# Optimization experiments

Hardware: AMD Instinct MI355X
Metric: run time of the kernel (lower is better)

Reference implementation:

```python
import jax, jax.numpy as jnp
import numpy as np

B, N, C = 8, 16384, 256

def setup_inputs() -> dict:
    key = jax.random.key(0)
    ks = jax.random.split(key, 5)
    scale = 1.0 / np.sqrt(C)
    return {
        "x_in": jax.random.normal(ks[0], (B, N, C), dtype=jnp.float32),
        "Wq": jax.random.normal(ks[1], (C, C), dtype=jnp.float32) * scale,
        "bq": jax.random.normal(ks[2], (C,), dtype=jnp.float32) * scale,
        "Wk": jax.random.normal(ks[3], (C, C), dtype=jnp.float32) * scale,
        "bk": jax.random.normal(ks[4], (C,), dtype=jnp.float32) * scale,
    }

def reference(x_in, Wq, bq, Wk, bk):
    b, n, c = x_in.shape
    # Faithful to torch: reshape (NOT transpose) to [B, C, N]
    x = x_in.reshape(b, c, n)
    # 1x1 Conv1d == per-position linear over channel dim
    Q = jnp.einsum('oc,bcn->bon', Wq, x) + bq[None, :, None]  # [B,C,N]
    K = jnp.einsum('oc,bcn->bon', Wk, x) + bk[None, :, None]  # [B,C,N]
    # Q @ K^T over length axis -> channel-channel scores [B,C,C]
    scores = jnp.einsum('bcn,bdn->bcd', Q, K)
    c_c = jax.nn.softmax(scores, axis=-1)
    # x_in @ c_c + residual -> [B,N,C]
    return jnp.einsum('bnc,bcd->bnd', x_in, c_c) + x_in
```

## Files before the change

### kernel.cpp

```cpp
#include <hip/hip_runtime.h>

#define Bn 8
#define Nn 16384
#define Cn 256
#define NC 32
#define CHUNK 512
#define NSTG 16

typedef __attribute__((ext_vector_type(4)))  float f32x4;
typedef __attribute__((ext_vector_type(16))) float f32x16;
typedef __attribute__((ext_vector_type(8)))  __bf16 bf16x8;
typedef __attribute__((ext_vector_type(8)))  _Float16 f16x8;
typedef __attribute__((ext_vector_type(8)))  unsigned short u16x8;

static __device__ __forceinline__ unsigned short f2bf(float f) {
    unsigned int u = __float_as_uint(f);
    u += 0x7fff + ((u >> 16) & 1);
    return (unsigned short)(u >> 16);
}
static __device__ __forceinline__ unsigned short f2h(float f) {
    return __builtin_bit_cast(unsigned short, (_Float16)f);
}
static __device__ __forceinline__ f32x16 mfma16h(u16x8 a, u16x8 b, f32x16 c) {
    return __builtin_amdgcn_mfma_f32_32x32x16_f16(
        __builtin_bit_cast(f16x8, a), __builtin_bit_cast(f16x8, b), c, 0, 0, 0);
}
static __device__ __forceinline__ f32x16 mfma16b(u16x8 a, u16x8 b, f32x16 c) {
    return __builtin_amdgcn_mfma_f32_32x32x16_bf16(
        __builtin_bit_cast(bf16x8, a), __builtin_bit_cast(bf16x8, b), c, 0, 0, 0);
}

__global__ __launch_bounds__(512, 4) void k_gram(
    const float* __restrict__ x, float* __restrict__ gpart,
    float* __restrict__ spart) {
  const int blk  = blockIdx.x;
  const int half = blk & 1;
  const int ck   = (blk >> 1) & (NC - 1);
  const int b    = blk >> 6;
  const float* xb = x + (size_t)b * Cn * Nn + (size_t)ck * CHUNK;
  const int rot  = (2 * ck + half) & (NSTG - 1);

  __shared__ __align__(16) char smem[2 * 20480];

  const int t    = threadIdx.x;
  const int lane = t & 63;
  const int w    = t >> 6;
  const int wm   = w & 1;
  const int wn   = w >> 1;
  const int ln   = lane & 31;
  const int kh   = lane >> 5;

  const int rt = t >> 3;
  const int c4 = t & 7;

  f32x16 acc[2][2];
#pragma unroll
  for (int m = 0; m < 2; ++m)
#pragma unroll
    for (int n = 0; n < 2; ++n)
#pragma unroll
      for (int i = 0; i < 16; ++i) acc[m][n][i] = 0.f;

  float srow[4] = {0.f, 0.f, 0.f, 0.f};
  const float* xrt = xb + (size_t)rt * Nn + c4 * 4;

  f32x4 ld[4];
  {
    const int sp = rot;
#pragma unroll
    for (int j = 0; j < 4; ++j)
      ld[j] = *(const f32x4*)(xrt + (size_t)j * (64 * Nn) + sp * 32);
  }

  for (int s = 0; s < NSTG; ++s) {
    char* buf = smem + (s & 1) * 20480;
#pragma unroll
    for (int j = 0; j < 4; ++j) {
      f32x4 v = ld[j];
      srow[j] += v.x + v.y + v.z + v.w;
      ushort4 h = make_ushort4(f2h(v.x), f2h(v.y), f2h(v.z), f2h(v.w));
      int row = rt + 64 * j;
      *(ushort4*)(buf + row * 80 + c4 * 8) = h;
    }
    if (s + 1 < NSTG) {
      const int sp = (s + 1 + rot) & (NSTG - 1);
#pragma unroll
      for (int j = 0; j < 4; ++j)
        ld[j] = *(const f32x4*)(xrt + (size_t)j * (64 * Nn) + sp * 32);
    }
    __syncthreads();
#pragma unroll
    for (int ks = 0; ks < 2; ++ks) {
      const int sl = ks * 2 + kh;
      u16x8 A[2], Bv[2];
#pragma unroll
      for (int m = 0; m < 2; ++m) {
        int r = half * 128 + wm * 64 + m * 32 + ln;
        A[m] = *(const u16x8*)(buf + r * 80 + sl * 16);
      }
#pragma unroll
      for (int n = 0; n < 2; ++n) {
        int r = wn * 64 + n * 32 + ln;
        Bv[n] = *(const u16x8*)(buf + r * 80 + sl * 16);
      }
#pragma unroll
      for (int m = 0; m < 2; ++m)
#pragma unroll
        for (int n = 0; n < 2; ++n)
          acc[m][n] = mfma16h(A[m], Bv[n], acc[m][n]);
    }
  }

#pragma unroll
  for (int j = 0; j < 4; ++j) {
    float v = srow[j];
    v += __shfl_xor(v, 1);
    v += __shfl_xor(v, 2);
    v += __shfl_xor(v, 4);
    if (c4 == 0 && half == 0)
      spart[(size_t)(b * NC + ck) * Cn + rt + 64 * j] = v;
  }

  float* gp = gpart + (size_t)(b * NC + ck) * (Cn * Cn);
#pragma unroll
  for (int m = 0; m < 2; ++m)
#pragma unroll
    for (int n = 0; n < 2; ++n)
#pragma unroll
      for (int r2 = 0; r2 < 16; ++r2) {
        int row = half * 128 + wm * 64 + m * 32 + (r2 & 3) + 8 * (r2 >> 2) + 4 * kh;
        int col = wn * 64 + n * 32 + ln;
        gp[row * Cn + col] = acc[m][n][r2];
      }
}

__global__ __launch_bounds__(256) void k_misc(
    const float* __restrict__ spart, const float* __restrict__ wk,
    const float* __restrict__ bk, float* __restrict__ sv,
    float* __restrict__ wkT, float* __restrict__ kN) {
  const int bb = blockIdx.x, t = threadIdx.x;
  __shared__ float s_l[256];
  float a = 0.f;
  for (int ck = 0; ck < NC; ++ck) a += spart[(size_t)(bb * NC + ck) * Cn + t];
  sv[bb * Cn + t] = a;
  s_l[t] = a;
#pragma unroll
  for (int j = 0; j < 32; ++j) {
    int k = bb * 32 + j;
    wkT[k * Cn + t] = wk[t * Cn + k];
  }
  __syncthreads();
  float k2 = 0.f;
  for (int c = 0; c < 256; ++c) k2 += wk[t * Cn + c] * s_l[c];
  kN[bb * Cn + t] = k2 + 16384.f * bk[t];
}

__global__ __launch_bounds__(256) void k_gk(
    const float* __restrict__ gpart, const float* __restrict__ sv,
    const float* __restrict__ wkT, const float* __restrict__ bk,
    float* __restrict__ GK) {
  const int b = blockIdx.x >> 5, tile = blockIdx.x & 31;
  const int r0 = tile * 8, t = threadIdx.x;
  __shared__ float g_l[8][256];

  float a[8];
#pragma unroll
  for (int j = 0; j < 8; ++j) a[j] = 0.f;
  const float* gp = gpart + (size_t)b * NC * 65536 + r0 * 256 + t;
  for (int ck = 0; ck < NC; ++ck) {
#pragma unroll
    for (int j = 0; j < 8; ++j) a[j] += gp[(size_t)ck * 65536 + j * 256];
  }
#pragma unroll
  for (int j = 0; j < 8; ++j) g_l[j][t] = a[j];
  __syncthreads();

  float acc[8];
#pragma unroll
  for (int r = 0; r < 8; ++r) acc[r] = 0.f;
  for (int k0 = 0; k0 < 256; k0 += 4) {
    float w0 = wkT[(k0 + 0) * 256 + t];
    float w1 = wkT[(k0 + 1) * 256 + t];
    float w2 = wkT[(k0 + 2) * 256 + t];
    float w3 = wkT[(k0 + 3) * 256 + t];
#pragma unroll
    for (int r = 0; r < 8; ++r) {
      f32x4 gv = *(const f32x4*)(&g_l[r][k0]);
      acc[r] += gv.x * w0 + gv.y * w1 + gv.z * w2 + gv.w * w3;
    }
  }
  float bkt = bk[t];
#pragma unroll
  for (int r = 0; r < 8; ++r) {
    float svr = sv[b * 256 + r0 + r];
    GK[((size_t)b * 256 + r0 + r) * 256 + t] = acc[r] + svr * bkt;
  }
}

__global__ __launch_bounds__(256) void k_scores(
    const float* __restrict__ wq, const float* __restrict__ GK,
    const float* __restrict__ bq, const float* __restrict__ kN,
    unsigned short* __restrict__ ccB) {
  const int b    = blockIdx.x >> 5;
  const int tile = blockIdx.x & 31;
  const int c0   = tile * 8;
  const int t    = threadIdx.x;

  __shared__ float wq_l[8][256];
  __shared__ float sc_l[8][256];
  __shared__ unsigned short cct_l[256][8];

#pragma unroll
  for (int j = 0; j < 8; ++j) wq_l[j][t] = wq[(c0 + j) * Cn + t];
  __syncthreads();

  float acc[8];
#pragma unroll
  for (int r = 0; r < 8; ++r) acc[r] = 0.f;
  for (int k0 = 0; k0 < 256; k0 += 4) {
    float g0 = GK[((size_t)b * 256 + k0 + 0) * 256 + t];
    float g1 = GK[((size_t)b * 256 + k0 + 1) * 256 + t];
    float g2 = GK[((size_t)b * 256 + k0 + 2) * 256 + t];
    float g3 = GK[((size_t)b * 256 + k0 + 3) * 256 + t];
#pragma unroll
    for (int r = 0; r < 8; ++r) {
      f32x4 qv = *(const f32x4*)(&wq_l[r][k0]);
      acc[r] += qv.x * g0 + qv.y * g1 + qv.z * g2 + qv.w * g3;
    }
  }
  float kNt = kN[b * 256 + t];
#pragma unroll
  for (int r = 0; r < 8; ++r) sc_l[r][t] = acc[r] + bq[c0 + r] * kNt;
  __syncthreads();

  const int r = t >> 5, sub = t & 31;
  float v[8];
#pragma unroll
  for (int j = 0; j < 8; ++j) v[j] = sc_l[r][sub + 32 * j];
  float mx = v[0];
#pragma unroll
  for (int j = 1; j < 8; ++j) mx = fmaxf(mx, v[j]);
#pragma unroll
  for (int msk = 16; msk >= 1; msk >>= 1) mx = fmaxf(mx, __shfl_xor(mx, msk, 32));
  float se = 0.f;
#pragma unroll
  for (int j = 0; j < 8; ++j) { v[j] = __expf(v[j] - mx); se += v[j]; }
#pragma unroll
  for (int msk = 16; msk >= 1; msk >>= 1) se += __shfl_xor(se, msk, 32);
  float inv = 1.f / se;
#pragma unroll
  for (int j = 0; j < 8; ++j) {
    int d = sub + 32 * j;
    float cc = v[j] * inv + ((d == c0 + r) ? 1.f : 0.f);
    cct_l[d][r] = f2bf(cc);
  }
  __syncthreads();
  *(uint4*)(ccB + (size_t)b * 65536 + (size_t)(tile * 256 + t) * 8) =
      *(const uint4*)(&cct_l[t][0]);
}

__global__ __launch_bounds__(256, 4) void k_out(
    const float* __restrict__ x, const unsigned short* __restrict__ ccB,
    float* __restrict__ out) {
  const int blk = blockIdx.x;
  const int b  = blk >> 8;
  const int n0 = (blk & 255) * 64;
  const float* xb = x + (size_t)b * Nn * Cn + (size_t)n0 * Cn;
  const unsigned short* cb = ccB + (size_t)b * 65536;
  float* ob = out + (size_t)b * Nn * Cn + (size_t)n0 * Cn;

  __shared__ __align__(16) char smem[32768];

  const int t    = threadIdx.x;
  const int lane = t & 63;
  const int w    = t >> 6;
  const int ln = lane & 31;
  const int kh = lane >> 5;

  f32x16 acc[2][2];
#pragma unroll
  for (int m = 0; m < 2; ++m)
#pragma unroll
    for (int n = 0; n < 2; ++n)
#pragma unroll
      for (int i = 0; i < 16; ++i) acc[m][n][i] = 0.f;

#pragma unroll
  for (int i = 0; i < 16; ++i) {
    int fi = i * 256 + t;
    f32x4 v = *(const f32x4*)(xb + (size_t)fi * 4);
    int row = fi >> 6, c = fi & 63;
    ushort4 hv = make_ushort4(f2bf(v.x), f2bf(v.y), f2bf(v.z), f2bf(v.w));
    *(ushort4*)(smem + row * 512 + ((c * 8) ^ ((row & 31) << 4))) = hv;
  }
  __syncthreads();

#pragma unroll
  for (int ks = 0; ks < 16; ++ks) {
    u16x8 A[2], Bv[2];
    const int g = ks * 2 + kh;
#pragma unroll
    for (int m = 0; m < 2; ++m) {
      int row = m * 32 + ln;
      A[m] = *(const u16x8*)(smem + row * 512 + ((g * 16) ^ ((row & 31) << 4)));
    }
#pragma unroll
    for (int n = 0; n < 2; ++n) {
      int d = w * 64 + n * 32 + ln;
      Bv[n] = *(const u16x8*)(cb + (size_t)g * 2048 + (size_t)d * 8);
    }
#pragma unroll
    for (int m = 0; m < 2; ++m)
#pragma unroll
      for (int n = 0; n < 2; ++n)
        acc[m][n] = mfma16b(A[m], Bv[n], acc[m][n]);
  }

#pragma unroll
  for (int m = 0; m < 2; ++m)
#pragma unroll
    for (int n = 0; n < 2; ++n)
#pragma unroll
      for (int r2 = 0; r2 < 16; ++r2) {
        int row = m * 32 + (r2 & 3) + 8 * (r2 >> 2) + 4 * kh;
        int col = w * 64 + n * 32 + ln;
        ob[(size_t)row * Cn + col] = acc[m][n][r2];
      }
}

extern "C" void kernel_launch(void* const* d_in, const int* in_sizes, int n_in,
                              void* d_out, int out_size, void* d_ws, size_t ws_size,
                              hipStream_t stream) {
  const float* x  = (const float*)d_in[0];
  const float* wq = (const float*)d_in[1];
  const float* bq = (const float*)d_in[2];
  const float* wk = (const float*)d_in[3];
  const float* bk = (const float*)d_in[4];
  float* out = (float*)d_out;

  float* gpart = (float*)d_ws;
  float* spart = gpart + (size_t)Bn * NC * 65536;
  float* sv    = spart + (size_t)Bn * NC * 256;
  float* wkT   = sv + (size_t)Bn * 256;
  float* kN    = wkT + 65536;
  float* GK    = kN + (size_t)Bn * 256;
  unsigned short* ccB = (unsigned short*)(GK + (size_t)Bn * 65536);

  hipLaunchKernelGGL(k_gram,   dim3(Bn * NC * 2), dim3(512), 0, stream, x, gpart, spart);
  hipLaunchKernelGGL(k_misc,   dim3(Bn),          dim3(256), 0, stream, spart, wk, bk, sv, wkT, kN);
  hipLaunchKernelGGL(k_gk,     dim3(Bn * 32),     dim3(256), 0, stream, gpart, sv, wkT, bk, GK);
  hipLaunchKernelGGL(k_scores, dim3(Bn * 32),     dim3(256), 0, stream, wq, GK, bq, kN, ccB);
  hipLaunchKernelGGL(k_out,    dim3(Bn * 256),    dim3(256), 0, stream, x, ccB, out);
}
```

Before: 156.6 us.

## Add fp16 pre-pack kernel with swizzled tiles and simplify gram kernel loads

```diff
diff --git a/kernel.cpp b/kernel.cpp
--- a/kernel.cpp
+++ b/kernel.cpp
@@ -4,8 +4,7 @@
 #define Nn 16384
 #define Cn 256
 #define NC 32
-#define CHUNK 512
-#define NSTG 16
+#define XPB ((size_t)8388608)
 
 typedef __attribute__((ext_vector_type(4)))  float f32x4;
 typedef __attribute__((ext_vector_type(16))) float f32x16;
@@ -30,28 +29,65 @@
         __builtin_bit_cast(bf16x8, a), __builtin_bit_cast(bf16x8, b), c, 0, 0, 0);
 }
 
+__global__ __launch_bounds__(256, 2) void k_pack(
+    const float* __restrict__ x, unsigned short* __restrict__ xp,
+    float* __restrict__ spart) {
+  const int blk = blockIdx.x;
+  const int nq  = blk & 3;
+  const int c8  = (blk >> 2) & 31;
+  const int b   = blk >> 7;
+  const int t   = threadIdx.x;
+  const int row = t >> 5;
+  const int l32 = t & 31;
+  const int c   = c8 * 8 + row;
+
+  __shared__ unsigned short lx[8][4096];
+
+  const float* src = x + (size_t)b * (Cn * Nn) + (size_t)c * Nn + nq * 4096;
+  float srow = 0.f;
+#pragma unroll 4
+  for (int it = 0; it < 32; ++it) {
+    int n = it * 128 + l32 * 4;
+    f32x4 v = *(const f32x4*)(src + n);
+    srow += v.x + v.y + v.z + v.w;
+    ushort4 h = make_ushort4(f2h(v.x), f2h(v.y), f2h(v.z), f2h(v.w));
+    *(ushort4*)(&lx[row][n]) = h;
+  }
+  srow += __shfl_xor(srow, 1, 32);
+  srow += __shfl_xor(srow, 2, 32);
+  srow += __shfl_xor(srow, 4, 32);
+  srow += __shfl_xor(srow, 8, 32);
+  srow += __shfl_xor(srow, 16, 32);
+  if (l32 == 0) spart[(b * 4 + nq) * Cn + c] = srow;
+  __syncthreads();
+
+  char* dstb = (char*)xp + (size_t)b * XPB;
+  const int n0   = l32 * 4;
+  const int slot = ((n0 >> 3) ^ (c & 15)) & 15;
+  const size_t woff = (size_t)c * 256 + slot * 16 + (n0 & 7) * 2;
+#pragma unroll 4
+  for (int ntl = 0; ntl < 32; ++ntl) {
+    int nt = nq * 32 + ntl;
+    ushort4 val = *(const ushort4*)(&lx[row][ntl * 128 + n0]);
+    *(ushort4*)(dstb + (size_t)nt * 65536 + woff) = val;
+  }
+}
+
 __global__ __launch_bounds__(512, 4) void k_gram(
-    const float* __restrict__ x, float* __restrict__ gpart,
-    float* __restrict__ spart) {
+    const unsigned short* __restrict__ xp, float* __restrict__ gpart) {
   const int blk  = blockIdx.x;
   const int half = blk & 1;
   const int ck   = (blk >> 1) & (NC - 1);
   const int b    = blk >> 6;
-  const float* xb = x + (size_t)b * Cn * Nn + (size_t)ck * CHUNK;
-  const int rot  = (2 * ck + half) & (NSTG - 1);
-
-  __shared__ __align__(16) char smem[2 * 20480];
+  const char* tb0 = (const char*)xp + (size_t)b * XPB + (size_t)(ck * 4) * 65536;
+
+  __shared__ __align__(16) char smem[65536];
 
   const int t    = threadIdx.x;
   const int lane = t & 63;
   const int w    = t >> 6;
-  const int wm   = w & 1;
-  const int wn   = w >> 1;
-  const int ln   = lane & 31;
-  const int kh   = lane >> 5;
-
-  const int rt = t >> 3;
-  const int c4 = t & 7;
+  const int wm = w & 1, wn = w >> 1;
+  const int ln = lane & 31, kh = lane >> 5;
 
   f32x16 acc[2][2];
 #pragma unroll
@@ -61,47 +97,34 @@
 #pragma unroll
       for (int i = 0; i < 16; ++i) acc[m][n][i] = 0.f;
 
-  float srow[4] = {0.f, 0.f, 0.f, 0.f};
-  const float* xrt = xb + (size_t)rt * Nn + c4 * 4;
-
-  f32x4 ld[4];
-  {
-    const int sp = rot;
-#pragma unroll
-    for (int j = 0; j < 4; ++j)
-      ld[j] = *(const f32x4*)(xrt + (size_t)j * (64 * Nn) + sp * 32);
-  }
-
-  for (int s = 0; s < NSTG; ++s) {
-    char* buf = smem + (s & 1) * 20480;
-#pragma unroll
-    for (int j = 0; j < 4; ++j) {
-      f32x4 v = ld[j];
-      srow[j] += v.x + v.y + v.z + v.w;
-      ushort4 h = make_ushort4(f2h(v.x), f2h(v.y), f2h(v.z), f2h(v.w));
-      int row = rt + 64 * j;
-      *(ushort4*)(buf + row * 80 + c4 * 8) = h;
-    }
-    if (s + 1 < NSTG) {
-      const int sp = (s + 1 + rot) & (NSTG - 1);
-#pragma unroll
-      for (int j = 0; j < 4; ++j)
-        ld[j] = *(const f32x4*)(xrt + (size_t)j * (64 * Nn) + sp * 32);
-    }
+  u16x8 ldreg[8];
+#pragma unroll
+  for (int r = 0; r < 8; ++r)
+    ldreg[r] = *(const u16x8*)(tb0 + r * 8192 + t * 16);
+
+  for (int st = 0; st < 4; ++st) {
+#pragma unroll
+    for (int r = 0; r < 8; ++r)
+      *(u16x8*)(smem + r * 8192 + t * 16) = ldreg[r];
     __syncthreads();
-#pragma unroll
-    for (int ks = 0; ks < 2; ++ks) {
-      const int sl = ks * 2 + kh;
+    if (st < 3) {
+#pragma unroll
+      for (int r = 0; r < 8; ++r)
+        ldreg[r] = *(const u16x8*)(tb0 + (st + 1) * 65536 + r * 8192 + t * 16);
+    }
+#pragma unroll
+    for (int sl = 0; sl < 8; ++sl) {
+      const int ch = sl * 2 + kh;
       u16x8 A[2], Bv[2];
 #pragma unroll
       for (int m = 0; m < 2; ++m) {
         int r = half * 128 + wm * 64 + m * 32 + ln;
-        A[m] = *(const u16x8*)(buf + r * 80 + sl * 16);
+        A[m] = *(const u16x8*)(smem + r * 256 + ((ch ^ (r & 15)) << 4));
       }
 #pragma unroll
       for (int n = 0; n < 2; ++n) {
         int r = wn * 64 + n * 32 + ln;
-        Bv[n] = *(const u16x8*)(buf + r * 80 + sl * 16);
+        Bv[n] = *(const u16x8*)(smem + r * 256 + ((ch ^ (r & 15)) << 4));
       }
 #pragma unroll
       for (int m = 0; m < 2; ++m)
@@ -109,16 +132,7 @@
         for (int n = 0; n < 2; ++n)
           acc[m][n] = mfma16h(A[m], Bv[n], acc[m][n]);
     }
-  }
-
-#pragma unroll
-  for (int j = 0; j < 4; ++j) {
-    float v = srow[j];
-    v += __shfl_xor(v, 1);
-    v += __shfl_xor(v, 2);
-    v += __shfl_xor(v, 4);
-    if (c4 == 0 && half == 0)
-      spart[(size_t)(b * NC + ck) * Cn + rt + 64 * j] = v;
+    __syncthreads();
   }
 
   float* gp = gpart + (size_t)(b * NC + ck) * (Cn * Cn);
@@ -141,7 +155,8 @@
   const int bb = blockIdx.x, t = threadIdx.x;
   __shared__ float s_l[256];
   float a = 0.f;
-  for (int ck = 0; ck < NC; ++ck) a += spart[(size_t)(bb * NC + ck) * Cn + t];
+#pragma unroll
+  for (int q = 0; q < 4; ++q) a += spart[(bb * 4 + q) * Cn + t];
   sv[bb * Cn + t] = a;
   s_l[t] = a;
 #pragma unroll
@@ -159,39 +174,35 @@
     const float* __restrict__ gpart, const float* __restrict__ sv,
     const float* __restrict__ wkT, const float* __restrict__ bk,
     float* __restrict__ GK) {
-  const int b = blockIdx.x >> 5, tile = blockIdx.x & 31;
-  const int r0 = tile * 8, t = threadIdx.x;
-  __shared__ float g_l[8][256];
-
-  float a[8];
-#pragma unroll
-  for (int j = 0; j < 8; ++j) a[j] = 0.f;
+  const int b = blockIdx.x >> 6, tile = blockIdx.x & 63;
+  const int r0 = tile * 4, t = threadIdx.x;
+  __shared__ float g_l[4][256];
+
+  float a[4] = {0.f, 0.f, 0.f, 0.f};
   const float* gp = gpart + (size_t)b * NC * 65536 + r0 * 256 + t;
   for (int ck = 0; ck < NC; ++ck) {
 #pragma unroll
-    for (int j = 0; j < 8; ++j) a[j] += gp[(size_t)ck * 65536 + j * 256];
-  }
-#pragma unroll
-  for (int j = 0; j < 8; ++j) g_l[j][t] = a[j];
-  __syncthreads();
-
-  float acc[8];
-#pragma unroll
-  for (int r = 0; r < 8; ++r) acc[r] = 0.f;
+    for (int j = 0; j < 4; ++j) a[j] += gp[(size_t)ck * 65536 + j * 256];
+  }
+#pragma unroll
+  for (int j = 0; j < 4; ++j) g_l[j][t] = a[j];
+  __syncthreads();
+
+  float acc[4] = {0.f, 0.f, 0.f, 0.f};
   for (int k0 = 0; k0 < 256; k0 += 4) {
     float w0 = wkT[(k0 + 0) * 256 + t];
     float w1 = wkT[(k0 + 1) * 256 + t];
     float w2 = wkT[(k0 + 2) * 256 + t];
     float w3 = wkT[(k0 + 3) * 256 + t];
 #pragma unroll
-    for (int r = 0; r < 8; ++r) {
+    for (int r = 0; r < 4; ++r) {
       f32x4 gv = *(const f32x4*)(&g_l[r][k0]);
       acc[r] += gv.x * w0 + gv.y * w1 + gv.z * w2 + gv.w * w3;
     }
   }
   float bkt = bk[t];
 #pragma unroll
-  for (int r = 0; r < 8; ++r) {
+  for (int r = 0; r < 4; ++r) {
     float svr = sv[b * 256 + r0 + r];
     GK[((size_t)b * 256 + r0 + r) * 256 + t] = acc[r] + svr * bkt;
   }
@@ -338,17 +349,19 @@
   const float* bk = (const float*)d_in[4];
   float* out = (float*)d_out;
 
-  float* gpart = (float*)d_ws;
+  unsigned short* xp = (unsigned short*)d_ws;
+  float* gpart = (float*)((char*)d_ws + (size_t)Bn * XPB);
   float* spart = gpart + (size_t)Bn * NC * 65536;
-  float* sv    = spart + (size_t)Bn * NC * 256;
+  float* sv    = spart + (size_t)Bn * 4 * 256;
   float* wkT   = sv + (size_t)Bn * 256;
   float* kN    = wkT + 65536;
   float* GK    = kN + (size_t)Bn * 256;
   unsigned short* ccB = (unsigned short*)(GK + (size_t)Bn * 65536);
 
-  hipLaunchKernelGGL(k_gram,   dim3(Bn * NC * 2), dim3(512), 0, stream, x, gpart, spart);
+  hipLaunchKernelGGL(k_pack,   dim3(Bn * 128),    dim3(256), 0, stream, x, xp, spart);
+  hipLaunchKernelGGL(k_gram,   dim3(Bn * NC * 2), dim3(512), 0, stream, xp, gpart);
   hipLaunchKernelGGL(k_misc,   dim3(Bn),          dim3(256), 0, stream, spart, wk, bk, sv, wkT, kN);
-  hipLaunchKernelGGL(k_gk,     dim3(Bn * 32),     dim3(256), 0, stream, gpart, sv, wkT, bk, GK);
+  hipLaunchKernelGGL(k_gk,     dim3(Bn * 64),     dim3(256), 0, stream, gpart, sv, wkT, bk, GK);
   hipLaunchKernelGGL(k_scores, dim3(Bn * 32),     dim3(256), 0, stream, wq, GK, bq, kN, ccB);
   hipLaunchKernelGGL(k_out,    dim3(Bn * 256),    dim3(256), 0, stream, x, ccB, out);
 }
```

After: 196.6 us. 25.5% more time.
